# Kernel optimization log

Hardware: AMD Instinct MI355X
Metric: run time of the kernel (lower is better)

## Reference

```python
import jax, jax.numpy as jnp
import numpy as np

NUM_HEADS = 12
EPS = 1e-6


def softmax_with_policy(attn, policy, eps=EPS):
    # attn: [B, H, N, N]; policy: [B, N, 1]
    B, H, N, _ = attn.shape
    attn_policy = policy.reshape(B, 1, 1, N)
    eye = jnp.eye(N, dtype=attn_policy.dtype).reshape(1, 1, N, N)
    attn_policy = attn_policy + (1.0 - attn_policy) * eye
    max_att = jnp.max(attn, axis=-1, keepdims=True)
    a = jnp.exp((attn - max_att).astype(jnp.float32)) * attn_policy.astype(jnp.float32)
    a = (a + eps / N) / (jnp.sum(a, axis=-1, keepdims=True) + eps)
    return a.astype(attn.dtype)


def setup_inputs() -> dict:
    key = jax.random.key(0)
    k1, k2, k3 = jax.random.split(key, 3)
    B, N, C = 16, 1024, 768
    x = jax.random.normal(k1, (B, N, C), dtype=jnp.float32)
    policy = jax.random.uniform(k2, (B, N, 1), dtype=jnp.float32)
    w_qkv = jax.random.normal(k3, (3 * C, C), dtype=jnp.float32) * (C ** -0.5)
    w_proj = jax.random.normal(jax.random.fold_in(key, 7), (C, C), dtype=jnp.float32) * (C ** -0.5)
    b_proj = jnp.zeros((C,), dtype=jnp.float32)
    return {"x": x, "policy": policy, "w_qkv": w_qkv, "w_proj": w_proj, "b_proj": b_proj, "sampler": 0}


def reference(x, policy, w_qkv, w_proj, b_proj, sampler):
    B, N, C = x.shape
    H = NUM_HEADS
    hd = C // H
    scale = hd ** -0.5
    qkv = (x @ w_qkv.T).reshape(B, N, 3, H, hd)
    qkv = jnp.transpose(qkv, (2, 0, 3, 1, 4))  # [3, B, H, N, hd]
    q, k, v = qkv[0], qkv[1], qkv[2]
    attn = jnp.einsum('bhnd,bhmd->bhnm', q, k) * scale
    attn = softmax_with_policy(attn, policy)
    out = jnp.einsum('bhnm,bhmd->bhnd', attn, v)
    out = jnp.transpose(out, (0, 2, 1, 3)).reshape(B, N, C)
    return out @ w_proj.T + b_proj
```

## Files before the change

### kernel.cpp

```cpp
#include <hip/hip_runtime.h>


#define NB 16
#define NN 1024
#define NC 768
#define NH 12
#define HD 64
#define NM (NB*NN)
#define QKVC (3*NC)
#define QSCALE 0.18033688011112042f
#define PSTR 68

typedef _Float16 f16;
typedef _Float16 f16x8 __attribute__((ext_vector_type(8)));
typedef _Float16 f16x4 __attribute__((ext_vector_type(4)));
typedef __fp16 fp16x2 __attribute__((ext_vector_type(2)));
typedef float f32x4 __attribute__((ext_vector_type(4)));

#if __has_builtin(__builtin_amdgcn_exp2f)
#define EXP2(x) __builtin_amdgcn_exp2f(x)
#else
#define EXP2(x) exp2f(x)
#endif

#define MFMA16(a,b,c) __builtin_amdgcn_mfma_f32_16x16x32_f16((a),(b),(c),0,0,0)
#define SCHED_FENCE() __builtin_amdgcn_sched_barrier(0)

__device__ inline f16x8 as_f16x8(uint4 u){
  union { uint4 u; f16x8 h; } v; v.u = u; return v.h;
}

__device__ inline void gl_lds16(const f16* g, f16* l){
  __builtin_amdgcn_global_load_lds(
      (const __attribute__((address_space(1))) void*)g,
      (__attribute__((address_space(3))) void*)l, 16, 0, 0);
}

__global__ void cvt_f32_f16(const float* __restrict__ in, f16* __restrict__ out, int n4){
  int i = blockIdx.x*blockDim.x + threadIdx.x;
  if (i < n4){
    float4 v = ((const float4*)in)[i];
    f16x4 h; h[0]=(f16)v.x; h[1]=(f16)v.y; h[2]=(f16)v.z; h[3]=(f16)v.w;
    ((f16x4*)out)[i] = h;
  }
}

__launch_bounds__(256)
__global__ void gemm_qkv(const f16* __restrict__ X, const f16* __restrict__ W,
                         f16* __restrict__ Q, f16* __restrict__ K, f16* __restrict__ VT){
  __shared__ f16 sA[128*32];
  __shared__ f16 sB[128*32];
  const int R0 = blockIdx.y*128, C0 = blockIdx.x*128;
  const int t = threadIdx.x;
  const int w = t >> 6, l = t & 63, quad = l >> 4, lr = l & 15;
  const int wr = w >> 1, wc = w & 1;
  const int row0 = t >> 2, kc0 = (t & 3)*8;
  f32x4 acc[4][4] = {};
  for (int bk = 0; bk < NC; bk += 32){
#pragma unroll
    for (int r = 0; r < 2; r++){
      int row = r*64 + row0;
      gl_lds16(X + (size_t)(R0 + row)*NC + bk + kc0, sA + r*2048 + w*512);
      gl_lds16(W + (size_t)(C0 + row)*NC + bk + kc0, sB + r*2048 + w*512);
    }
    __syncthreads();
    f16x8 af[4], bf[4];
#pragma unroll
    for (int mt = 0; mt < 4; mt++)
      af[mt] = as_f16x8(*(const uint4*)(sA + (wr*64 + mt*16 + lr)*32 + quad*8));
#pragma unroll
    for (int nt = 0; nt < 4; nt++)
      bf[nt] = as_f16x8(*(const uint4*)(sB + (wc*64 + nt*16 + lr)*32 + quad*8));
#pragma unroll
    for (int mt = 0; mt < 4; mt++)
#pragma unroll
      for (int nt = 0; nt < 4; nt++)
        acc[mt][nt] = MFMA16(af[mt], bf[nt], acc[mt][nt]);
    __syncthreads();
  }
  const int type = C0 / NC;
#pragma unroll
  for (int nt = 0; nt < 4; nt++){
    int colg = C0 + wc*64 + nt*16 + lr;
    int rem  = colg - type*NC;
    int hh = rem >> 6, d = rem & 63;
#pragma unroll
    for (int mt = 0; mt < 4; mt++)
#pragma unroll
      for (int i = 0; i < 4; i++){
        int row = R0 + wr*64 + mt*16 + quad*4 + i;
        int bb = row >> 10, np = row & 1023;
        int bh = bb*NH + hh;
        float a = acc[mt][nt][i];
        if (type == 0)      Q[(bh << 16) + (np << 6) + d] = (f16)(a * QSCALE);
        else if (type == 1) K[(bh << 16) + (np << 6) + d] = (f16)a;
        else                VT[(bh << 16) + (d << 10) + np] = (f16)a;
      }
  }
}

__global__ void vsum_kernel(const f16* __restrict__ VT, float* __restrict__ vsum){
  int bh = blockIdx.x;
  int t = threadIdx.x;
  int row = t >> 2, part = t & 3;
  const uint4* p = (const uint4*)(VT + ((size_t)bh << 16) + row*NN + part*256);
  float s = 0.f;
#pragma unroll
  for (int i = 0; i < 32; i++){
    f16x8 v = as_f16x8(p[i]);
#pragma unroll
    for (int j = 0; j < 8; j++) s += (float)v[j];
  }
  __shared__ float sR[64][4];
  sR[row][part] = s;
  __syncthreads();
  if (t < 64) vsum[bh*64 + t] = sR[t][0] + sR[t][1] + sR[t][2] + sR[t][3];
}


#define STAGE(BUF, KEY0H)                                                     \
  _Pragma("unroll")                                                           \
  for (int j = 0; j < 2; j++){                                                \
    const int s_  = j*256 + t;                                                \
    const int r_  = s_ >> 3;                                                  \
    const int sl_ = (s_ & 7) ^ (r_ & 7);                                      \
    f16* du_ = (f16*)&sK[BUF][(j*256 + (t & 192))*8];                         \
    f16* dv_ = (f16*)&sVT[BUF][(j*256 + (t & 192))*8];                        \
    gl_lds16(Kg  + (size_t)((KEY0H) + r_)*HD + sl_*8, du_);                   \
    gl_lds16(VTg + (size_t)r_*NN + (KEY0H) + sl_*8,   dv_);                   \
  }

__launch_bounds__(256, 3)
__global__ void attn_kernel(const f16* __restrict__ Q, const f16* __restrict__ K,
                            const f16* __restrict__ VT, const float* __restrict__ policy,
                            const float* __restrict__ vsum, f16* __restrict__ O){
  __shared__ f16 sK[2][4096];
  __shared__ f16 sVT[2][4096];
  __shared__ f16 sP[4][2][16][PSTR];
  __shared__ float sPol[1024];

  const int blk = blockIdx.x;
  const int bh = blk % (NB*NH);
  const int qt = blk / (NB*NH);
  const int b = bh / NH;
  const size_t base = (size_t)bh << 16;

  const int t = threadIdx.x;
  const int w = t >> 6, l = t & 63, quad = l >> 4, lr = l & 15;
  const int q0 = qt*128 + w*32;
  const int qrow = q0 + lr;
  const int h = bh - b*NH;
  const int xr = lr & 7;
  const int kx0 = (quad ^ xr)*8;
  const int kx1 = ((4 + quad) ^ xr)*8;

  *(float4*)&sPol[t*4] = *(const float4*)(policy + b*NN + t*4);

  f16x8 qf[2][2];
#pragma unroll
  for (int tq = 0; tq < 2; tq++)
#pragma unroll
    for (int hf = 0; hf < 2; hf++)
      qf[tq][hf] = as_f16x8(*(const uint4*)(Q + base + (size_t)(q0 + tq*16 + lr)*HD + hf*32 + quad*8));

  float vs[4];
#pragma unroll
  for (int nt = 0; nt < 4; nt++) vs[nt] = vsum[bh*64 + nt*16 + lr];

  f16x8 ones;
#pragma unroll
  for (int j = 0; j < 8; j++) ones[j] = (f16)1.0f;

  float m_run[2] = {-INFINITY, -INFINITY};
  f32x4 acc_l[2] = {};
  f32x4 o[2][4] = {};

  const f16* Kg  = K + base;
  const f16* VTg = VT + base;

  STAGE(0, 0);
  asm volatile("s_waitcnt vmcnt(0) lgkmcnt(0)" ::: "memory");
  SCHED_FENCE();
  __builtin_amdgcn_s_barrier();
  SCHED_FENCE();

#pragma unroll 1
  for (int hs = 0; hs < 16; hs++){
    const int cur = hs & 1;
    const int key0h = hs*64;
    if (hs < 15){
      STAGE(cur^1, key0h + 64);
      asm volatile("s_waitcnt vmcnt(4)" ::: "memory");
    } else {
      asm volatile("s_waitcnt vmcnt(0)" ::: "memory");
    }
    SCHED_FENCE();
    __builtin_amdgcn_s_barrier();
    SCHED_FENCE();

    const f16* sKc = (const f16*)sK[cur];
    const f16* sVc = (const f16*)sVT[cur];

    f32x4 accA[4], accB[4];
#pragma unroll
    for (int ct = 0; ct < 4; ct++){ accA[ct] = (f32x4){0,0,0,0}; accB[ct] = (f32x4){0,0,0,0}; }
    __builtin_amdgcn_s_setprio(1);
#pragma unroll
    for (int ct = 0; ct < 4; ct++){
      const f16* kp = sKc + (ct*16 + lr)*64;
      f16x8 k0 = as_f16x8(*(const uint4*)(kp + kx0));
      f16x8 k1 = as_f16x8(*(const uint4*)(kp + kx1));
      accA[ct] = MFMA16(k0, qf[0][0], accA[ct]);
      accA[ct] = MFMA16(k1, qf[0][1], accA[ct]);
      accB[ct] = MFMA16(k0, qf[1][0], accB[ct]);
      accB[ct] = MFMA16(k1, qf[1][1], accB[ct]);
    }
    __builtin_amdgcn_s_setprio(0);

    {
      float mA = m_run[0], mB = m_run[1];
      const bool diag = (hs == 2*qt + (w >> 1));
      if (!diag){
#pragma unroll
        for (int ct = 0; ct < 4; ct++){
          const int kb = ct*16 + quad*4;
          float4 pol4 = *(const float4*)&sPol[key0h + kb];
          const float* p4 = (const float*)&pol4;
          mA = fmaxf(mA, fmaxf(fmaxf(accA[ct][0], accA[ct][1]), fmaxf(accA[ct][2], accA[ct][3])));
          mB = fmaxf(mB, fmaxf(fmaxf(accB[ct][0], accB[ct][1]), fmaxf(accB[ct][2], accB[ct][3])));
          union { f16x4 v; fp16x2 h[2]; } uA, uB;
          uA.h[0] = __builtin_amdgcn_cvt_pkrtz(EXP2(accA[ct][0])*p4[0], EXP2(accA[ct][1])*p4[1]);
          uA.h[1] = __builtin_amdgcn_cvt_pkrtz(EXP2(accA[ct][2])*p4[2], EXP2(accA[ct][3])*p4[3]);
          uB.h[0] = __builtin_amdgcn_cvt_pkrtz(EXP2(accB[ct][0])*p4[0], EXP2(accB[ct][1])*p4[1]);
          uB.h[1] = __builtin_amdgcn_cvt_pkrtz(EXP2(accB[ct][2])*p4[2], EXP2(accB[ct][3])*p4[3]);
          *(f16x4*)&sP[w][0][lr][kb] = uA.v;
          *(f16x4*)&sP[w][1][lr][kb] = uB.v;
        }
      } else {
#pragma unroll
        for (int ct = 0; ct < 4; ct++){
          const int kb = ct*16 + quad*4;
          float4 pol4 = *(const float4*)&sPol[key0h + kb];
          const float* p4 = (const float*)&pol4;
          float eA[4], eB[4];
#pragma unroll
          for (int i2 = 0; i2 < 4; i2++){
            int kg = key0h + kb + i2;
            float polA = (kg == qrow)      ? 1.0f : p4[i2];
            float polB = (kg == qrow + 16) ? 1.0f : p4[i2];
            mA = fmaxf(mA, accA[ct][i2]); mB = fmaxf(mB, accB[ct][i2]);
            eA[i2] = EXP2(accA[ct][i2]) * polA;
            eB[i2] = EXP2(accB[ct][i2]) * polB;
          }
          union { f16x4 v; fp16x2 h[2]; } uA, uB;
          uA.h[0] = __builtin_amdgcn_cvt_pkrtz(eA[0], eA[1]);
          uA.h[1] = __builtin_amdgcn_cvt_pkrtz(eA[2], eA[3]);
          uB.h[0] = __builtin_amdgcn_cvt_pkrtz(eB[0], eB[1]);
          uB.h[1] = __builtin_amdgcn_cvt_pkrtz(eB[2], eB[3]);
          *(f16x4*)&sP[w][0][lr][kb] = uA.v;
          *(f16x4*)&sP[w][1][lr][kb] = uB.v;
        }
      }
      m_run[0] = mA; m_run[1] = mB;
    }

    __builtin_amdgcn_s_setprio(1);
#pragma unroll
    for (int s8g = 0; s8g < 2; s8g++){
      f16x8 pfA = as_f16x8(*(const uint4*)&sP[w][0][lr][s8g*32 + quad*8]);
      f16x8 pfB = as_f16x8(*(const uint4*)&sP[w][1][lr][s8g*32 + quad*8]);
      acc_l[0] = MFMA16(pfA, ones, acc_l[0]);
      acc_l[1] = MFMA16(pfB, ones, acc_l[1]);
      const int sx = ((s8g*4 + quad) ^ xr)*8;
#pragma unroll
      for (int nt = 0; nt < 4; nt++){
        f16x8 vf = as_f16x8(*(const uint4*)(sVc + (nt*16 + lr)*64 + sx));
        o[0][nt] = MFMA16(pfA, vf, o[0][nt]);
        o[1][nt] = MFMA16(pfB, vf, o[1][nt]);
      }
    }
    __builtin_amdgcn_s_setprio(0);
    SCHED_FENCE();
    __builtin_amdgcn_s_barrier();
    SCHED_FENCE();
  }

#pragma unroll
  for (int tq = 0; tq < 2; tq++){
    float mq = m_run[tq];
    mq = fmaxf(mq, __shfl_xor(mq, 16));
    mq = fmaxf(mq, __shfl_xor(mq, 32));
#pragma unroll
    for (int i = 0; i < 4; i++){
      float mi = __shfl(mq, quad*4 + i);
      float E  = EXP2(mi);
      float li = acc_l[tq][i];
      float inv = 1.0f / (li + 1e-6f*E);
      float ec  = (1e-6f/1024.0f)*E;
      int row = q0 + tq*16 + quad*4 + i;
      f16* op = O + (size_t)(b*NN + row)*NC + h*HD;
#pragma unroll
      for (int nt = 0; nt < 4; nt++)
        op[nt*16 + lr] = (f16)((o[tq][nt][i] + ec*vs[nt]) * inv);
    }
  }
}

__launch_bounds__(256)
__global__ void gemm_proj(const f16* __restrict__ A, const f16* __restrict__ W,
                          const float* __restrict__ bias, float* __restrict__ out){
  __shared__ f16 sA[128*32];
  __shared__ f16 sB[128*32];
  const int R0 = blockIdx.y*128, C0 = blockIdx.x*128;
  const int t = threadIdx.x;
  const int w = t >> 6, l = t & 63, quad = l >> 4, lr = l & 15;
  const int wr = w >> 1, wc = w & 1;
  const int row0 = t >> 2, kc0 = (t & 3)*8;
  f32x4 acc[4][4] = {};
  for (int bk = 0; bk < NC; bk += 32){
#pragma unroll
    for (int r = 0; r < 2; r++){
      int row = r*64 + row0;
      gl_lds16(A + (size_t)(R0 + row)*NC + bk + kc0, sA + r*2048 + w*512);
      gl_lds16(W + (size_t)(C0 + row)*NC + bk + kc0, sB + r*2048 + w*512);
    }
    __syncthreads();
    f16x8 af[4], bf[4];
#pragma unroll
    for (int mt = 0; mt < 4; mt++)
      af[mt] = as_f16x8(*(const uint4*)(sA + (wr*64 + mt*16 + lr)*32 + quad*8));
#pragma unroll
    for (int nt = 0; nt < 4; nt++)
      bf[nt] = as_f16x8(*(const uint4*)(sB + (wc*64 + nt*16 + lr)*32 + quad*8));
#pragma unroll
    for (int mt = 0; mt < 4; mt++)
#pragma unroll
      for (int nt = 0; nt < 4; nt++)
        acc[mt][nt] = MFMA16(af[mt], bf[nt], acc[mt][nt]);
    __syncthreads();
  }
#pragma unroll
  for (int nt = 0; nt < 4; nt++){
    int colg = C0 + wc*64 + nt*16 + lr;
    float bv = bias[colg];
#pragma unroll
    for (int mt = 0; mt < 4; mt++)
#pragma unroll
      for (int i = 0; i < 4; i++){
        int row = R0 + wr*64 + mt*16 + quad*4 + i;
        out[(size_t)row*NC + colg] = acc[mt][nt][i] + bv;
      }
  }
}

extern "C" void kernel_launch(void* const* d_in, const int* in_sizes, int n_in,
                              void* d_out, int out_size, void* d_ws, size_t ws_size,
                              hipStream_t stream) {
  const float* x      = (const float*)d_in[0];
  const float* policy = (const float*)d_in[1];
  const float* w_qkv  = (const float*)d_in[2];
  const float* w_proj = (const float*)d_in[3];
  const float* b_proj = (const float*)d_in[4];
  float* out = (float*)d_out;

  f16* x_h     = (f16*)d_ws;
  f16* wqkv_h  = x_h + (size_t)NM*NC;
  f16* wproj_h = wqkv_h + (size_t)QKVC*NC;
  f16* q_h     = wproj_h + (size_t)NC*NC;
  f16* k_h     = q_h + (size_t)NM*NC;
  f16* vt_h    = k_h + (size_t)NM*NC;
  float* vsum_f = (float*)(vt_h + (size_t)NM*NC);
  f16* attn_h  = x_h;

  cvt_f32_f16<<<(NM*NC/4 + 255)/256, 256, 0, stream>>>(x, x_h, NM*NC/4);
  cvt_f32_f16<<<(QKVC*NC/4 + 255)/256, 256, 0, stream>>>(w_qkv, wqkv_h, QKVC*NC/4);
  cvt_f32_f16<<<(NC*NC/4 + 255)/256, 256, 0, stream>>>(w_proj, wproj_h, NC*NC/4);

  gemm_qkv<<<dim3(QKVC/128, NM/128), 256, 0, stream>>>(x_h, wqkv_h, q_h, k_h, vt_h);

  vsum_kernel<<<dim3(NB*NH), 256, 0, stream>>>(vt_h, vsum_f);

  attn_kernel<<<dim3(NB*NH*(NN/128)), 256, 0, stream>>>(q_h, k_h, vt_h, policy, vsum_f, attn_h);

  gemm_proj<<<dim3(NC/128, NM/128), 256, 0, stream>>>(attn_h, wproj_h, b_proj, out);
}
```

Measured before the change: 368.3 us.

## Double-buffer GEMM LDS loads and merge three conversion kernels into one

Both projection GEMMs now use two LDS buffers, prefetching the next K-slice via global_load_lds while computing on the current one. Explicit vmcnt waits, raw barriers and MFMA priority raising replace the plain __syncthreads loop. The three fp32-to-fp16 conversion launches are merged into one kernel that dispatches by index range, saving launch overhead. Doubling LDS use per block may reduce occupancy, and the hand-placed waitcnt counts must match the number of outstanding loads.

New measurement: 344.6 us. -6.4%, faster.

```diff
diff --git a/kernel.cpp b/kernel.cpp
--- a/kernel.cpp
+++ b/kernel.cpp
@@ -36,48 +36,79 @@
       (__attribute__((address_space(3))) void*)l, 16, 0, 0);
 }
 
-__global__ void cvt_f32_f16(const float* __restrict__ in, f16* __restrict__ out, int n4){
+#define CVT_N1 (NM*NC/4)
+#define CVT_N2 (QKVC*NC/4)
+#define CVT_N3 (NC*NC/4)
+__global__ void cvt_all(const float* __restrict__ x, const float* __restrict__ wq,
+                        const float* __restrict__ wp, f16* __restrict__ xh,
+                        f16* __restrict__ wqh, f16* __restrict__ wph){
   int i = blockIdx.x*blockDim.x + threadIdx.x;
-  if (i < n4){
-    float4 v = ((const float4*)in)[i];
-    f16x4 h; h[0]=(f16)v.x; h[1]=(f16)v.y; h[2]=(f16)v.z; h[3]=(f16)v.w;
-    ((f16x4*)out)[i] = h;
-  }
-}
+  const float* in; f16* out; int j;
+  if (i < CVT_N1){ in = x; out = xh; j = i; }
+  else if (i < CVT_N1 + CVT_N2){ in = wq; out = wqh; j = i - CVT_N1; }
+  else { in = wp; out = wph; j = i - CVT_N1 - CVT_N2; }
+  float4 v = ((const float4*)in)[j];
+  f16x4 h; h[0]=(f16)v.x; h[1]=(f16)v.y; h[2]=(f16)v.z; h[3]=(f16)v.w;
+  ((f16x4*)out)[j] = h;
+}
+
+#define GEMM_STAGE(SRC_A, SRC_B, BUF, BK)                                     \
+  _Pragma("unroll")                                                           \
+  for (int r = 0; r < 2; r++){                                                \
+    int row = r*64 + row0;                                                    \
+    gl_lds16(SRC_A + (size_t)(R0 + row)*NC + (BK) + kc0, sA[BUF] + r*2048 + w*512); \
+    gl_lds16(SRC_B + (size_t)(C0 + row)*NC + (BK) + kc0, sB[BUF] + r*2048 + w*512); \
+  }
+
+#define GEMM_PIPELINE(SRC_A, SRC_B)                                           \
+  GEMM_STAGE(SRC_A, SRC_B, 0, 0);                                             \
+  asm volatile("s_waitcnt vmcnt(0)" ::: "memory");                            \
+  SCHED_FENCE();                                                              \
+  __builtin_amdgcn_s_barrier();                                               \
+  SCHED_FENCE();                                                              \
+  _Pragma("unroll 1")                                                         \
+  for (int kt = 0; kt < 24; kt++){                                            \
+    const int cur = kt & 1;                                                   \
+    if (kt < 23){                                                             \
+      GEMM_STAGE(SRC_A, SRC_B, cur^1, (kt+1)*32);                             \
+      asm volatile("s_waitcnt vmcnt(4)" ::: "memory");                        \
+    } else {                                                                  \
+      asm volatile("s_waitcnt vmcnt(0)" ::: "memory");                        \
+    }                                                                         \
+    SCHED_FENCE();                                                            \
+    __builtin_amdgcn_s_barrier();                                             \
+    SCHED_FENCE();                                                            \
+    f16x8 af[4], bf[4];                                                       \
+    _Pragma("unroll")                                                         \
+    for (int mt = 0; mt < 4; mt++)                                            \
+      af[mt] = as_f16x8(*(const uint4*)(sA[cur] + (wr*64 + mt*16 + lr)*32 + quad*8)); \
+    _Pragma("unroll")                                                         \
+    for (int nt = 0; nt < 4; nt++)                                            \
+      bf[nt] = as_f16x8(*(const uint4*)(sB[cur] + (wc*64 + nt*16 + lr)*32 + quad*8)); \
+    __builtin_amdgcn_s_setprio(1);                                            \
+    _Pragma("unroll")                                                         \
+    for (int mt = 0; mt < 4; mt++)                                            \
+      _Pragma("unroll")                                                       \
+      for (int nt = 0; nt < 4; nt++)                                          \
+        acc[mt][nt] = MFMA16(af[mt], bf[nt], acc[mt][nt]);                    \
+    __builtin_amdgcn_s_setprio(0);                                            \
+    SCHED_FENCE();                                                            \
+    __builtin_amdgcn_s_barrier();                                             \
+    SCHED_FENCE();                                                            \
+  }
 
 __launch_bounds__(256)
 __global__ void gemm_qkv(const f16* __restrict__ X, const f16* __restrict__ W,
                          f16* __restrict__ Q, f16* __restrict__ K, f16* __restrict__ VT){
-  __shared__ f16 sA[128*32];
-  __shared__ f16 sB[128*32];
+  __shared__ f16 sA[2][128*32];
+  __shared__ f16 sB[2][128*32];
   const int R0 = blockIdx.y*128, C0 = blockIdx.x*128;
   const int t = threadIdx.x;
   const int w = t >> 6, l = t & 63, quad = l >> 4, lr = l & 15;
   const int wr = w >> 1, wc = w & 1;
   const int row0 = t >> 2, kc0 = (t & 3)*8;
   f32x4 acc[4][4] = {};
-  for (int bk = 0; bk < NC; bk += 32){
-#pragma unroll
-    for (int r = 0; r < 2; r++){
-      int row = r*64 + row0;
-      gl_lds16(X + (size_t)(R0 + row)*NC + bk + kc0, sA + r*2048 + w*512);
-      gl_lds16(W + (size_t)(C0 + row)*NC + bk + kc0, sB + r*2048 + w*512);
-    }
-    __syncthreads();
-    f16x8 af[4], bf[4];
-#pragma unroll
-    for (int mt = 0; mt < 4; mt++)
-      af[mt] = as_f16x8(*(const uint4*)(sA + (wr*64 + mt*16 + lr)*32 + quad*8));
-#pragma unroll
-    for (int nt = 0; nt < 4; nt++)
-      bf[nt] = as_f16x8(*(const uint4*)(sB + (wc*64 + nt*16 + lr)*32 + quad*8));
-#pragma unroll
-    for (int mt = 0; mt < 4; mt++)
-#pragma unroll
-      for (int nt = 0; nt < 4; nt++)
-        acc[mt][nt] = MFMA16(af[mt], bf[nt], acc[mt][nt]);
-    __syncthreads();
-  }
+  GEMM_PIPELINE(X, W);
   const int type = C0 / NC;
 #pragma unroll
   for (int nt = 0; nt < 4; nt++){
@@ -116,7 +147,6 @@
   __syncthreads();
   if (t < 64) vsum[bh*64 + t] = sR[t][0] + sR[t][1] + sR[t][2] + sR[t][3];
 }
-
 
 #define STAGE(BUF, KEY0H)                                                     \
   _Pragma("unroll")                                                           \
@@ -309,36 +339,15 @@
 __launch_bounds__(256)
 __global__ void gemm_proj(const f16* __restrict__ A, const f16* __restrict__ W,
                           const float* __restrict__ bias, float* __restrict__ out){
-  __shared__ f16 sA[128*32];
-  __shared__ f16 sB[128*32];
+  __shared__ f16 sA[2][128*32];
+  __shared__ f16 sB[2][128*32];
   const int R0 = blockIdx.y*128, C0 = blockIdx.x*128;
   const int t = threadIdx.x;
   const int w = t >> 6, l = t & 63, quad = l >> 4, lr = l & 15;
   const int wr = w >> 1, wc = w & 1;
   const int row0 = t >> 2, kc0 = (t & 3)*8;
   f32x4 acc[4][4] = {};
-  for (int bk = 0; bk < NC; bk += 32){
-#pragma unroll
-    for (int r = 0; r < 2; r++){
-      int row = r*64 + row0;
-      gl_lds16(A + (size_t)(R0 + row)*NC + bk + kc0, sA + r*2048 + w*512);
-      gl_lds16(W + (size_t)(C0 + row)*NC + bk + kc0, sB + r*2048 + w*512);
-    }
-    __syncthreads();
-    f16x8 af[4], bf[4];
-#pragma unroll
-    for (int mt = 0; mt < 4; mt++)
-      af[mt] = as_f16x8(*(const uint4*)(sA + (wr*64 + mt*16 + lr)*32 + quad*8));
-#pragma unroll
-    for (int nt = 0; nt < 4; nt++)
-      bf[nt] = as_f16x8(*(const uint4*)(sB + (wc*64 + nt*16 + lr)*32 + quad*8));
-#pragma unroll
-    for (int mt = 0; mt < 4; mt++)
-#pragma unroll
-      for (int nt = 0; nt < 4; nt++)
-        acc[mt][nt] = MFMA16(af[mt], bf[nt], acc[mt][nt]);
-    __syncthreads();
-  }
+  GEMM_PIPELINE(A, W);
 #pragma unroll
   for (int nt = 0; nt < 4; nt++){
     int colg = C0 + wc*64 + nt*16 + lr;
@@ -372,9 +381,7 @@
   float* vsum_f = (float*)(vt_h + (size_t)NM*NC);
   f16* attn_h  = x_h;
 
-  cvt_f32_f16<<<(NM*NC/4 + 255)/256, 256, 0, stream>>>(x, x_h, NM*NC/4);
-  cvt_f32_f16<<<(QKVC*NC/4 + 255)/256, 256, 0, stream>>>(w_qkv, wqkv_h, QKVC*NC/4);
-  cvt_f32_f16<<<(NC*NC/4 + 255)/256, 256, 0, stream>>>(w_proj, wproj_h, NC*NC/4);
+  cvt_all<<<(CVT_N1+CVT_N2+CVT_N3)/256, 256, 0, stream>>>(x, w_qkv, w_proj, x_h, wqkv_h, wproj_h);
 
   gemm_qkv<<<dim3(QKVC/128, NM/128), 256, 0, stream>>>(x_h, wqkv_h, q_h, k_h, vt_h);
 
```
